# Kernel optimization log

Hardware: AMD Instinct MI355X
Metric: run time of the kernel (lower is better)

The kernel has to match this reference:

```python
import jax, jax.numpy as jnp
import numpy as np
import math

BATCH = 16384
N = 1024            # in_size == in_size_extended == out_size (power of 2)
M = 10              # log2(N) butterfly stages
NSTACK = 1


def setup_inputs() -> dict:
    key = jax.random.key(0)
    k_x, k_t, k_b = jax.random.split(key, 3)
    x = jax.random.normal(k_x, (BATCH, N), dtype=jnp.float32)
    # untied 'regular' init: randn * 1/sqrt(2)
    twiddle = jax.random.normal(k_t, (NSTACK, M, N // 2, 2, 2), dtype=jnp.float32) / jnp.sqrt(2.0).astype(jnp.float32)
    bound = 1.0 / math.sqrt(N)
    bias = jax.random.uniform(k_b, (N,), dtype=jnp.float32, minval=-bound, maxval=bound)
    return {"x": x, "twiddle": twiddle, "bias": bias}


def _butterfly_mult_untied(twiddle, x, increasing_stride=True):
    # twiddle: (nstack, m, n/2, 2, 2); x: (batch, nstack, n)
    batch, nstack, n = x.shape
    m = twiddle.shape[1]
    out = x
    stages = range(m) if increasing_stride else range(m - 1, -1, -1)
    for log_stride in stages:
        stride = 1 << log_stride
        nblk = n // (2 * stride)
        # t[s, k, r, i, j]: 2x2 factor for block k, within-block position r
        t = twiddle[:, log_stride].reshape(nstack, nblk, stride, 2, 2)
        xr = out.reshape(batch, nstack, nblk, 2, stride)
        # out[b,s,k,i,r] = sum_j t[s,k,r,i,j] * x[b,s,k,j,r]
        out = jnp.einsum('skrij,bskjr->bskir', t, xr).reshape(batch, nstack, n)
    return out


def reference(x, twiddle, bias):
    # nstack == 1, in_size == out_size == 2^m: no padding / averaging / slicing branches
    out = _butterfly_mult_untied(twiddle, x[:, None, :], increasing_stride=True)
    out = out.reshape(x.shape[0], N)
    return out + bias
```

## Files before the change

### kernel.cpp

```cpp
#include <hip/hip_runtime.h>


#define BATCH 16384
#define NCOL 1024
#define RPW 4
#define TWS_BYTES (10 * 8 * 64 * 16)

__global__ __launch_bounds__(64) void repack_tw(
    const float* __restrict__ tw, float4* __restrict__ ws)
{
    const int s = blockIdx.x;
    const int lane = threadIdx.x;
    const float4* raw4 = reinterpret_cast<const float4*>(tw + s * 2048);
    const float2* raw2 = reinterpret_cast<const float2*>(tw + s * 2048);

    #pragma unroll
    for (int k = 0; k < 8; ++k) {
        float4 val;
        if (s < 2) {
            const int eh = k >> 1, j = k & 1;
            val = raw4[eh * 128 + lane * 2 + j];
        } else if (s < 8) {
            const int b = s - 2, m = 1 << b;
            const int i = (lane >> b) & 1;
            const int lp = ((lane >> (b + 1)) << b) | (lane & (m - 1));
            const int eh = k >> 1, ep = k & 1;
            float2 a = raw2[(eh * 128 + lp * 4 + 2 * ep) * 2 + i];
            float2 c = raw2[(eh * 128 + lp * 4 + 2 * ep + 1) * 2 + i];
            val = make_float4(a.x, a.y, c.x, c.y);
        } else {
            const int g = k >> 2, el = k & 3;
            val = raw4[g * 256 + lane * 4 + el];
        }
        ws[(s * 8 + k) * 64 + lane] = val;
    }
}

__global__ __launch_bounds__(256, 2) void butterfly_kernel(
    const float* __restrict__ x,
    const float4* __restrict__ tws,
    const float* __restrict__ bias,
    float* __restrict__ out)
{
    const int lane = threadIdx.x & 63;
    const int wave_in_block = threadIdx.x >> 6;
    const int gwave = blockIdx.x * 4 + wave_in_block;
    const int row0 = gwave * RPW;

    float v[RPW][4][4];

    const float4* x4 = reinterpret_cast<const float4*>(x);
    #pragma unroll
    for (int q = 0; q < RPW; ++q) {
        #pragma unroll
        for (int eh = 0; eh < 4; ++eh) {
            float4 t = x4[(row0 + q) * 256 + eh * 64 + lane];
            v[q][eh][0] = t.x; v[q][eh][1] = t.y;
            v[q][eh][2] = t.z; v[q][eh][3] = t.w;
        }
    }

    #pragma unroll
    for (int k = 0; k < 8; ++k) {
        const float4 T = tws[(0 * 8 + k) * 64 + lane];
        const int eh = k >> 1, j = k & 1;
        #pragma unroll
        for (int q = 0; q < RPW; ++q) {
            const float a = v[q][eh][2 * j];
            const float b = v[q][eh][2 * j + 1];
            v[q][eh][2 * j]     = T.x * a + T.y * b;
            v[q][eh][2 * j + 1] = T.z * a + T.w * b;
        }
    }

    #pragma unroll
    for (int k = 0; k < 8; ++k) {
        const float4 T = tws[(1 * 8 + k) * 64 + lane];
        const int eh = k >> 1, j = k & 1;
        #pragma unroll
        for (int q = 0; q < RPW; ++q) {
            const float a = v[q][eh][j];
            const float b = v[q][eh][j + 2];
            v[q][eh][j]     = T.x * a + T.y * b;
            v[q][eh][j + 2] = T.z * a + T.w * b;
        }
    }

    #pragma unroll
    for (int s = 2; s < 8; ++s) {
        const int b = s - 2;
        const int m = 1 << b;
        const int i = (lane >> b) & 1;
        float4 T[8];
        #pragma unroll
        for (int k = 0; k < 8; ++k) T[k] = tws[(s * 8 + k) * 64 + lane];
        #pragma unroll
        for (int q = 0; q < RPW; ++q) {
            #pragma unroll
            for (int k = 0; k < 8; ++k) {
                const int eh = k >> 1, ep = k & 1;
                {
                    const float own = v[q][eh][2 * ep];
                    const float p = __shfl_xor(own, m, 64);
                    const float x0 = i ? p : own;
                    const float x1 = i ? own : p;
                    v[q][eh][2 * ep] = T[k].x * x0 + T[k].y * x1;
                }
                {
                    const float own = v[q][eh][2 * ep + 1];
                    const float p = __shfl_xor(own, m, 64);
                    const float x0 = i ? p : own;
                    const float x1 = i ? own : p;
                    v[q][eh][2 * ep + 1] = T[k].z * x0 + T[k].w * x1;
                }
            }
        }
    }

    #pragma unroll
    for (int k = 0; k < 8; ++k) {
        const float4 T = tws[(8 * 8 + k) * 64 + lane];
        const int g = k >> 2, el = k & 3;
        #pragma unroll
        for (int q = 0; q < RPW; ++q) {
            const float a = v[q][2 * g][el];
            const float b = v[q][2 * g + 1][el];
            v[q][2 * g][el]     = T.x * a + T.y * b;
            v[q][2 * g + 1][el] = T.z * a + T.w * b;
        }
    }

    #pragma unroll
    for (int k = 0; k < 8; ++k) {
        const float4 T = tws[(9 * 8 + k) * 64 + lane];
        const int h = k >> 2, el = k & 3;
        #pragma unroll
        for (int q = 0; q < RPW; ++q) {
            const float a = v[q][h][el];
            const float b = v[q][h + 2][el];
            v[q][h][el]     = T.x * a + T.y * b;
            v[q][h + 2][el] = T.z * a + T.w * b;
        }
    }

    float4* o4 = reinterpret_cast<float4*>(out);
    const float4* b4 = reinterpret_cast<const float4*>(bias);
    #pragma unroll
    for (int eh = 0; eh < 4; ++eh) {
        const float4 bb = b4[eh * 64 + lane];
        #pragma unroll
        for (int q = 0; q < RPW; ++q) {
            float4 t;
            t.x = v[q][eh][0] + bb.x;
            t.y = v[q][eh][1] + bb.y;
            t.z = v[q][eh][2] + bb.z;
            t.w = v[q][eh][3] + bb.w;
            o4[(row0 + q) * 256 + eh * 64 + lane] = t;
        }
    }
}

__global__ __launch_bounds__(256) void butterfly_fallback(
    const float* __restrict__ x,
    const float* __restrict__ tw,
    const float* __restrict__ bias,
    float* __restrict__ out)
{
    const int lane = threadIdx.x & 63;
    const int wave_in_block = threadIdx.x >> 6;
    const int gwave = blockIdx.x * 4 + wave_in_block;
    const int row0 = gwave * 2;

    float v[2][4][4];
    const float4* x4 = reinterpret_cast<const float4*>(x);
    #pragma unroll
    for (int q = 0; q < 2; ++q)
        #pragma unroll
        for (int eh = 0; eh < 4; ++eh) {
            float4 t = x4[(row0 + q) * 256 + eh * 64 + lane];
            v[q][eh][0] = t.x; v[q][eh][1] = t.y;
            v[q][eh][2] = t.z; v[q][eh][3] = t.w;
        }

    #pragma unroll
    for (int s = 0; s < 2; ++s) {
        const float4* t4 = reinterpret_cast<const float4*>(tw + s * 2048);
        #pragma unroll
        for (int eh = 0; eh < 4; ++eh)
            #pragma unroll
            for (int j = 0; j < 2; ++j) {
                const float4 T = t4[eh * 128 + lane * 2 + j];
                #pragma unroll
                for (int q = 0; q < 2; ++q) {
                    const int a0 = (s == 0) ? 2 * j : j;
                    const int a1 = (s == 0) ? 2 * j + 1 : j + 2;
                    const float a = v[q][eh][a0];
                    const float b = v[q][eh][a1];
                    v[q][eh][a0] = T.x * a + T.y * b;
                    v[q][eh][a1] = T.z * a + T.w * b;
                }
            }
    }
    #pragma unroll
    for (int s = 2; s < 8; ++s) {
        const int b = s - 2, m = 1 << b;
        const int i = (lane >> b) & 1;
        const int lp = ((lane >> (b + 1)) << b) | (lane & (m - 1));
        const float2* t2 = reinterpret_cast<const float2*>(tw + s * 2048);
        float2 T[4][4];
        #pragma unroll
        for (int eh = 0; eh < 4; ++eh)
            #pragma unroll
            for (int el = 0; el < 4; ++el)
                T[eh][el] = t2[(eh * 128 + lp * 4 + el) * 2 + i];
        #pragma unroll
        for (int q = 0; q < 2; ++q)
            #pragma unroll
            for (int eh = 0; eh < 4; ++eh)
                #pragma unroll
                for (int el = 0; el < 4; ++el) {
                    const float own = v[q][eh][el];
                    const float p = __shfl_xor(own, m, 64);
                    const float x0 = i ? p : own;
                    const float x1 = i ? own : p;
                    v[q][eh][el] = T[eh][el].x * x0 + T[eh][el].y * x1;
                }
    }
    #pragma unroll
    for (int s = 8; s < 10; ++s) {
        const float4* t4 = reinterpret_cast<const float4*>(tw + s * 2048);
        #pragma unroll
        for (int g = 0; g < 2; ++g)
            #pragma unroll
            for (int el = 0; el < 4; ++el) {
                const float4 T = t4[g * 256 + lane * 4 + el];
                #pragma unroll
                for (int q = 0; q < 2; ++q) {
                    const int a0 = (s == 8) ? 2 * g : g;
                    const int a1 = (s == 8) ? 2 * g + 1 : g + 2;
                    const float a = v[q][a0][el];
                    const float b = v[q][a1][el];
                    v[q][a0][el] = T.x * a + T.y * b;
                    v[q][a1][el] = T.z * a + T.w * b;
                }
            }
    }
    float4* o4 = reinterpret_cast<float4*>(out);
    const float4* b4 = reinterpret_cast<const float4*>(bias);
    #pragma unroll
    for (int eh = 0; eh < 4; ++eh) {
        const float4 bb = b4[eh * 64 + lane];
        #pragma unroll
        for (int q = 0; q < 2; ++q) {
            float4 t;
            t.x = v[q][eh][0] + bb.x;
            t.y = v[q][eh][1] + bb.y;
            t.z = v[q][eh][2] + bb.z;
            t.w = v[q][eh][3] + bb.w;
            o4[(row0 + q) * 256 + eh * 64 + lane] = t;
        }
    }
}

extern "C" void kernel_launch(void* const* d_in, const int* in_sizes, int n_in,
                              void* d_out, int out_size, void* d_ws, size_t ws_size,
                              hipStream_t stream) {
    const float* x    = (const float*)d_in[0];
    const float* tw   = (const float*)d_in[1];
    const float* bias = (const float*)d_in[2];
    float* out = (float*)d_out;

    if (ws_size >= TWS_BYTES) {
        float4* tws = (float4*)d_ws;
        repack_tw<<<10, 64, 0, stream>>>(tw, tws);
        const int blocks = (BATCH / RPW) / 4;
        butterfly_kernel<<<blocks, 256, 0, stream>>>(x, tws, bias, out);
    } else {
        const int blocks = (BATCH / 2) / 4;
        butterfly_fallback<<<blocks, 256, 0, stream>>>(x, tw, bias, out);
    }
}
```

Before: 48.13 us.

## Use DPP lane swaps for small-stride shuffle stages and halve rows per wave

Replaces the ds_bpermute-based __shfl_xor for butterfly strides 1, 2 and 8 with DPP quad_perm and row_ror moves, which avoid the LDS crossbar round trip. Rows per wave drop from 4 to 2 and the min-blocks launch bound is removed, which changes register pressure, occupancy and the grid size. Fewer rows per wave means each wave loads twiddles for less work, which raises twiddle traffic per row. The row_ror:8 control for stride 8 relies on a 16-lane rotate by 8 being equivalent to xor 8.

```diff
diff --git a/kernel.cpp b/kernel.cpp
--- a/kernel.cpp
+++ b/kernel.cpp
@@ -3,8 +3,23 @@
 
 #define BATCH 16384
 #define NCOL 1024
-#define RPW 4
+#define RPW 2
 #define TWS_BYTES (10 * 8 * 64 * 16)
+
+template<int CTRL>
+__device__ __forceinline__ float fdpp(float x) {
+    int xi = __builtin_bit_cast(int, x);
+    int r = __builtin_amdgcn_update_dpp(0, xi, CTRL, 0xf, 0xf, false);
+    return __builtin_bit_cast(float, r);
+}
+
+template<int M>
+__device__ __forceinline__ float xpartner(float x) {
+    if constexpr (M == 1)       return fdpp<0xB1>(x);
+    else if constexpr (M == 2)  return fdpp<0x4E>(x);
+    else if constexpr (M == 8)  return fdpp<0x128>(x);
+    else                        return __shfl_xor(x, M, 64);
+}
 
 __global__ __launch_bounds__(64) void repack_tw(
     const float* __restrict__ tw, float4* __restrict__ ws)
@@ -36,7 +51,40 @@
     }
 }
 
-__global__ __launch_bounds__(256, 2) void butterfly_kernel(
+template<int S>
+__device__ __forceinline__ void shfl_stage(
+    float v[RPW][4][4], const float4* __restrict__ tws, int lane)
+{
+    constexpr int b = S - 2;
+    constexpr int m = 1 << b;
+    const int i = (lane >> b) & 1;
+    float4 T[8];
+    #pragma unroll
+    for (int k = 0; k < 8; ++k) T[k] = tws[(S * 8 + k) * 64 + lane];
+    #pragma unroll
+    for (int q = 0; q < RPW; ++q) {
+        #pragma unroll
+        for (int k = 0; k < 8; ++k) {
+            const int eh = k >> 1, ep = k & 1;
+            {
+                const float own = v[q][eh][2 * ep];
+                const float p = xpartner<m>(own);
+                const float x0 = i ? p : own;
+                const float x1 = i ? own : p;
+                v[q][eh][2 * ep] = T[k].x * x0 + T[k].y * x1;
+            }
+            {
+                const float own = v[q][eh][2 * ep + 1];
+                const float p = xpartner<m>(own);
+                const float x0 = i ? p : own;
+                const float x1 = i ? own : p;
+                v[q][eh][2 * ep + 1] = T[k].z * x0 + T[k].w * x1;
+            }
+        }
+    }
+}
+
+__global__ __launch_bounds__(256) void butterfly_kernel(
     const float* __restrict__ x,
     const float4* __restrict__ tws,
     const float* __restrict__ bias,
@@ -86,36 +134,12 @@
         }
     }
 
-    #pragma unroll
-    for (int s = 2; s < 8; ++s) {
-        const int b = s - 2;
-        const int m = 1 << b;
-        const int i = (lane >> b) & 1;
-        float4 T[8];
-        #pragma unroll
-        for (int k = 0; k < 8; ++k) T[k] = tws[(s * 8 + k) * 64 + lane];
-        #pragma unroll
-        for (int q = 0; q < RPW; ++q) {
-            #pragma unroll
-            for (int k = 0; k < 8; ++k) {
-                const int eh = k >> 1, ep = k & 1;
-                {
-                    const float own = v[q][eh][2 * ep];
-                    const float p = __shfl_xor(own, m, 64);
-                    const float x0 = i ? p : own;
-                    const float x1 = i ? own : p;
-                    v[q][eh][2 * ep] = T[k].x * x0 + T[k].y * x1;
-                }
-                {
-                    const float own = v[q][eh][2 * ep + 1];
-                    const float p = __shfl_xor(own, m, 64);
-                    const float x0 = i ? p : own;
-                    const float x1 = i ? own : p;
-                    v[q][eh][2 * ep + 1] = T[k].z * x0 + T[k].w * x1;
-                }
-            }
-        }
-    }
+    shfl_stage<2>(v, tws, lane);
+    shfl_stage<3>(v, tws, lane);
+    shfl_stage<4>(v, tws, lane);
+    shfl_stage<5>(v, tws, lane);
+    shfl_stage<6>(v, tws, lane);
+    shfl_stage<7>(v, tws, lane);
 
     #pragma unroll
     for (int k = 0; k < 8; ++k) {
```

Result: faster. 43.86 us (-8.9%).
